# Kernel tuning notes

Hardware: AMD Instinct MI355X
Metric: run time of the kernel (lower is better)

The kernel has to match this reference:

```python
import jax, jax.numpy as jnp
import numpy as np

BS, RES = 2, 512
H_LVL = RES // 2 + 1   # floor(512/2)+1 = 257
W_LVL = RES            # 512
NQ = H_LVL * W_LVL     # 131584
D, HEADS, PTS = 128, 8, 4
DH = D // HEADS


def setup_inputs() -> dict:
    key = jax.random.key(0)
    ks = jax.random.split(key, 9)
    s = 0.02  # weight init scale
    return {
        "query":   jax.random.normal(ks[0], (BS, NQ, D), jnp.float32),
        "W_value": jax.random.normal(ks[1], (D, D), jnp.float32) * s,
        "b_value": jax.random.normal(ks[2], (D,), jnp.float32) * s,
        "W_off":   jax.random.normal(ks[3], (D, HEADS * PTS * 2), jnp.float32) * s,
        "b_off":   jax.random.normal(ks[4], (HEADS * PTS * 2,), jnp.float32) * s,
        "W_attn":  jax.random.normal(ks[5], (D, HEADS * PTS), jnp.float32) * s,
        "b_attn":  jax.random.normal(ks[6], (HEADS * PTS,), jnp.float32) * s,
        "W_out":   jax.random.normal(ks[7], (D, D), jnp.float32) * s,
        "b_out":   jax.random.normal(ks[8], (D,), jnp.float32) * s,
    }


def _bilinear_zeros(V, x, y, H, W):
    """grid_sample(mode=bilinear, padding=zeros, align_corners=False) equivalent.
    V: [G, H*W, DH]; x, y: [G, S] pixel coords. Returns [G, S, DH]."""
    x0 = jnp.floor(x); y0 = jnp.floor(y)
    x0i = x0.astype(jnp.int32); y0i = y0.astype(jnp.int32)
    x1i = x0i + 1; y1i = y0i + 1
    wx1 = x - x0; wx0 = 1.0 - wx1
    wy1 = y - y0; wy0 = 1.0 - wy1

    def corner(xi, yi, w):
        valid = (xi >= 0) & (xi < W) & (yi >= 0) & (yi < H)
        idx = jnp.clip(yi, 0, H - 1) * W + jnp.clip(xi, 0, W - 1)
        val = jnp.take_along_axis(V, idx[:, :, None], axis=1)  # [G,S,DH]
        return (w * valid.astype(w.dtype))[:, :, None] * val

    return (corner(x0i, y0i, wx0 * wy0) + corner(x1i, y0i, wx1 * wy0)
            + corner(x0i, y1i, wx0 * wy1) + corner(x1i, y1i, wx1 * wy1))


def reference(query, W_value, b_value, W_off, b_off, W_attn, b_attn, W_out, b_out):
    B, NQ_, D_ = query.shape
    H, W = H_LVL, W_LVL

    # projections (mmcv MSDeformAttn)
    value = (query @ W_value + b_value).reshape(B, NQ_, HEADS, DH)
    offsets = (query @ W_off + b_off).reshape(B, NQ_, HEADS, PTS, 2)  # num_levels=1
    attn = jax.nn.softmax((query @ W_attn + b_attn).reshape(B, NQ_, HEADS, PTS), axis=-1)

    # reference points: meshgrid of normalized (col=x, row=y), row-major flatten
    gy, gx = jnp.meshgrid(jnp.linspace(0.0, 1.0, H), jnp.linspace(0.0, 1.0, W), indexing="ij")
    ref = jnp.stack([gx, gy], axis=-1).reshape(NQ_, 2).astype(query.dtype)  # [NQ,2]

    # sampling locations in [0,1]; offset normalizer = (W, H)
    norm = jnp.array([W, H], dtype=query.dtype)
    loc = ref[None, :, None, None, :] + offsets / norm  # [B,NQ,HEADS,PTS,2]

    # grid_sample align_corners=False: pixel = loc*size - 0.5
    x = loc[..., 0] * W - 0.5
    y = loc[..., 1] * H - 0.5

    G = B * HEADS
    V = value.transpose(0, 2, 1, 3).reshape(G, H * W, DH)          # [G,HW,DH]
    xs = x.transpose(0, 2, 1, 3).reshape(G, NQ_ * PTS)
    ys = y.transpose(0, 2, 1, 3).reshape(G, NQ_ * PTS)

    samp = _bilinear_zeros(V, xs, ys, H, W).reshape(B, HEADS, NQ_, PTS, DH)
    aw = attn.transpose(0, 2, 1, 3)                                 # [B,HEADS,NQ,PTS]
    out = jnp.einsum("bhqp,bhqpd->bqhd", aw, samp).reshape(B, NQ_, D_)
    out = out @ W_out + b_out

    # mmcv adds identity inside the attention module; outer forward adds residual again
    return out + query + query
```

## Files before the change

### kernel.cpp

```cpp
#include <hip/hip_runtime.h>
#include <hip/hip_bf16.h>

#define BS     2
#define H_LVL  257
#define W_LVL  512
#define NQC    (H_LVL * W_LVL)
#define DD     128
#define HEADS  8
#define PTS    4
#define DH     16
#define MTOT   (BS * NQC)

typedef float v4f __attribute__((ext_vector_type(4)));
typedef short v8s __attribute__((ext_vector_type(8)));

static __device__ __forceinline__ unsigned short f2bb(float f) {
    union { float f; unsigned int u; } v; v.f = f;
    const unsigned int u = v.u;
    return (unsigned short)((u + 0x7fffu + ((u >> 16) & 1u)) >> 16);
}
static __device__ __forceinline__ float bb2f(unsigned short h) {
    union { unsigned int u; float f; } v; v.u = ((unsigned int)h) << 16;
    return v.f;
}
static __device__ __forceinline__ void fma4(float4& acc, float w, const unsigned short* p) {
    const ushort4 r = *(const ushort4*)p;
    acc.x = fmaf(w, bb2f(r.x), acc.x);
    acc.y = fmaf(w, bb2f(r.y), acc.y);
    acc.z = fmaf(w, bb2f(r.z), acc.z);
    acc.w = fmaf(w, bb2f(r.w), acc.w);
}

__global__ __launch_bounds__(256) void prep_kernel(
    const float* __restrict__ Wv, const float* __restrict__ Woff,
    const float* __restrict__ Wattn, const float* __restrict__ Wout,
    const float* __restrict__ boff, const float* __restrict__ battn,
    unsigned short* __restrict__ WtV, unsigned short* __restrict__ Wt96,
    unsigned short* __restrict__ WtO, float* __restrict__ bcat)
{
    const int id = blockIdx.x * 256 + threadIdx.x;
    {
        const int n = id >> 7, k = id & 127;
        WtV[id] = f2bb(Wv[k * DD + n]);
        WtO[id] = f2bb(Wout[k * DD + n]);
    }
    if (id < 96 * 128) {
        const int n = id >> 7, k = id & 127;
        Wt96[id] = f2bb(n < 64 ? Woff[k * 64 + n] : Wattn[k * 32 + (n - 64)]);
    }
    if (id < 96) bcat[id] = (id < 64) ? boff[id] : battn[id - 64];
}

template<int NT, int MODE>
__global__ __launch_bounds__(256) void gemm_kernel(
    const float* __restrict__ A,
    const unsigned short* __restrict__ Wt,
    const float* __restrict__ bias,
    unsigned short* __restrict__ dst_bf,
    float* __restrict__ dst_f,
    const float* __restrict__ query)
{
    constexpr int NC = NT * 16;
    __shared__ unsigned short As[64 * 136];
    __shared__ unsigned short Ws[NC * 136];
    const int t = threadIdx.x;
    const long long m0 = (long long)blockIdx.x * 64;

    {
        const float4* src = (const float4*)(A + m0 * DD);
        #pragma unroll
        for (int rep = 0; rep < 8; ++rep) {
            const int c = rep * 256 + t;
            const int m = c >> 5, f4 = c & 31;
            const float4 v = src[c];
            ushort4 hq;
            hq.x = f2bb(v.x); hq.y = f2bb(v.y); hq.z = f2bb(v.z); hq.w = f2bb(v.w);
            *(ushort4*)(&As[m * 136 + f4 * 4]) = hq;
        }
    }
    {
        const uint4* src = (const uint4*)Wt;
        for (int c = t; c < NC * 16; c += 256) {
            const int n = c >> 4, kc = c & 15;
            *(uint4*)(&Ws[n * 136 + kc * 8]) = src[c];
        }
    }
    __syncthreads();

    const int lane = t & 63, wave = t >> 6;
    const int l15 = lane & 15, quad = lane >> 4;

    v4f acc[NT];
    #pragma unroll
    for (int nt = 0; nt < NT; ++nt) { v4f z = {0.f, 0.f, 0.f, 0.f}; acc[nt] = z; }

    const int arow = wave * 16 + l15;
    #pragma unroll
    for (int kk = 0; kk < 4; ++kk) {
        const v8s a = *(const v8s*)(&As[arow * 136 + kk * 32 + quad * 8]);
        #pragma unroll
        for (int nt = 0; nt < NT; ++nt) {
            const v8s b = *(const v8s*)(&Ws[(nt * 16 + l15) * 136 + kk * 32 + quad * 8]);
            acc[nt] = __builtin_amdgcn_mfma_f32_16x16x32_bf16(a, b, acc[nt], 0, 0, 0);
        }
    }

    const long long mbase = m0 + wave * 16 + quad * 4;
    if (MODE == 0) {
        const int b = (int)(m0 / NQC);
        #pragma unroll
        for (int nt = 0; nt < NT; ++nt) {
            const float bi = bias[nt * 16 + l15];
            #pragma unroll
            for (int r = 0; r < 4; ++r) {
                const long long q = (mbase + r) - (long long)b * NQC;
                dst_bf[((long long)(b * HEADS + nt) * NQC + q) * DH + l15] =
                    f2bb(acc[nt][r] + bi);
            }
        }
    } else if (MODE == 1) {
        #pragma unroll
        for (int nt = 0; nt < NT; ++nt) {
            const float bi = bias[nt * 16 + l15];
            #pragma unroll
            for (int r = 0; r < 4; ++r)
                dst_bf[(mbase + r) * 96 + nt * 16 + l15] = f2bb(acc[nt][r] + bi);
        }
    } else {
        #pragma unroll
        for (int nt = 0; nt < NT; ++nt) {
            const float bi = bias[nt * 16 + l15];
            #pragma unroll
            for (int r = 0; r < 4; ++r) {
                const long long idx = (mbase + r) * DD + nt * 16 + l15;
                dst_f[idx] = acc[nt][r] + bi + 2.0f * query[idx];
            }
        }
    }
}

template<bool PRECOMP>
__global__ __launch_bounds__(256) void sample2_kernel(
    const unsigned short* __restrict__ proj,
    const float* __restrict__ query,
    const float* __restrict__ Woff, const float* __restrict__ boff,
    const float* __restrict__ Wattn, const float* __restrict__ battn,
    const unsigned short* __restrict__ value,
    float* __restrict__ attn_out)
{
    __shared__ float projF[8][96];
    const int t = threadIdx.x;
    const long long qbase = (long long)blockIdx.x * 8;

    if constexpr (PRECOMP) {
        if (t < 192) {
            const ushort4 r = *(const ushort4*)(proj + qbase * 96 + t * 4);
            const int qq = (t * 4) / 96, c = (t * 4) % 96;
            projF[qq][c]     = bb2f(r.x);
            projF[qq][c + 1] = bb2f(r.y);
            projF[qq][c + 2] = bb2f(r.z);
            projF[qq][c + 3] = bb2f(r.w);
        }
        __syncthreads();
    } else {
        __shared__ float qs[8][DD];
        {
            const int qi = t >> 5, k4 = (t & 31) * 4;
            const float4 v = *(const float4*)(query + (qbase + qi) * DD + k4);
            qs[qi][k4] = v.x; qs[qi][k4 + 1] = v.y; qs[qi][k4 + 2] = v.z; qs[qi][k4 + 3] = v.w;
        }
        __syncthreads();
        for (int task = t; task < 768; task += 256) {
            const int qi = task / 96, c = task % 96;
            float a; const float* wp; int stride;
            if (c < 64) { a = boff[c];       wp = Woff  + c;        stride = 64; }
            else        { a = battn[c - 64]; wp = Wattn + (c - 64); stride = 32; }
            for (int k = 0; k < DD; ++k) a += qs[qi][k] * wp[k * stride];
            projF[qi][c] = a;
        }
        __syncthreads();
    }

    const int q_loc = t >> 5, lq = t & 31;
    const int h = lq >> 2, p_own = lq & 3;
    const long long bq = qbase + q_loc;
    const int b = (int)(bq / NQC);
    const int qidx = (int)(bq - (long long)b * NQC);
    const int row = qidx >> 9, col = qidx & 511;

    const float offx = projF[q_loc][(h * PTS + p_own) * 2];
    const float offy = projF[q_loc][(h * PTS + p_own) * 2 + 1];
    const float al   = projF[q_loc][64 + h * PTS + p_own];
    float mx = fmaxf(al, __shfl_xor(al, 1));
    mx = fmaxf(mx, __shfl_xor(mx, 2));
    const float e = __expf(al - mx);
    float sm = e + __shfl_xor(e, 1);
    sm += __shfl_xor(sm, 2);
    const float aw = e / sm;

    const float x = (float)col * (1.0f / 511.0f) * (float)W_LVL + offx - 0.5f;
    const float y = (float)row * (1.0f / 256.0f) * (float)H_LVL + offy - 0.5f;
    const float x0f = floorf(x), y0f = floorf(y);
    const int x0 = (int)x0f, y0 = (int)y0f;
    const int x1 = x0 + 1, y1 = y0 + 1;
    const float wx1 = x - x0f, wx0 = 1.0f - wx1;
    const float wy1 = y - y0f, wy0 = 1.0f - wy1;
    const float vx0 = (x0 >= 0 && x0 < W_LVL) ? 1.f : 0.f;
    const float vx1 = (x1 >= 0 && x1 < W_LVL) ? 1.f : 0.f;
    const float vy0 = (y0 >= 0 && y0 < H_LVL) ? 1.f : 0.f;
    const float vy1 = (y1 >= 0 && y1 < H_LVL) ? 1.f : 0.f;
    float w00 = aw * wx0 * wy0 * vx0 * vy0;
    float w01 = aw * wx1 * wy0 * vx1 * vy0;
    float w10 = aw * wx0 * wy1 * vx0 * vy1;
    float w11 = aw * wx1 * wy1 * vx1 * vy1;
    const int xc0 = min(max(x0, 0), W_LVL - 1), xc1 = min(max(x1, 0), W_LVL - 1);
    const int yc0 = min(max(y0, 0), H_LVL - 1), yc1 = min(max(y1, 0), H_LVL - 1);
    int i00 = yc0 * W_LVL + xc0, i01 = yc0 * W_LVL + xc1;
    int i10 = yc1 * W_LVL + xc0, i11 = yc1 * W_LVL + xc1;

    const int dq4 = p_own;
    const unsigned short* V = value + (size_t)(b * HEADS + h) * NQC * DH + dq4 * 4;
    float4 acc = {0.f, 0.f, 0.f, 0.f};
    const int lbase = (t & 63) & ~3;
    #pragma unroll
    for (int p = 0; p < 4; ++p) {
        const int src = lbase + p;
        const float W00 = __shfl(w00, src, 64), W01 = __shfl(w01, src, 64);
        const float W10 = __shfl(w10, src, 64), W11 = __shfl(w11, src, 64);
        const int   I00 = __shfl(i00, src, 64), I01 = __shfl(i01, src, 64);
        const int   I10 = __shfl(i10, src, 64), I11 = __shfl(i11, src, 64);
        fma4(acc, W00, V + (size_t)I00 * DH);
        fma4(acc, W01, V + (size_t)I01 * DH);
        fma4(acc, W10, V + (size_t)I10 * DH);
        fma4(acc, W11, V + (size_t)I11 * DH);
    }
    *(float4*)(attn_out + bq * DD + h * DH + dq4 * 4) = acc;
}

extern "C" void kernel_launch(void* const* d_in, const int* in_sizes, int n_in,
                              void* d_out, int out_size, void* d_ws, size_t ws_size,
                              hipStream_t stream) {
    const float* query = (const float*)d_in[0];
    const float* Wv    = (const float*)d_in[1];
    const float* bv    = (const float*)d_in[2];
    const float* Woff  = (const float*)d_in[3];
    const float* boff  = (const float*)d_in[4];
    const float* Wattn = (const float*)d_in[5];
    const float* battn = (const float*)d_in[6];
    const float* Wout  = (const float*)d_in[7];
    const float* bout  = (const float*)d_in[8];
    float* out = (float*)d_out;

    char* ws = (char*)d_ws;
    size_t off = 0;
    unsigned short* WtV  = (unsigned short*)(ws + off); off += 16384 * 2;
    unsigned short* Wt96 = (unsigned short*)(ws + off); off += 12288 * 2;
    unsigned short* WtO  = (unsigned short*)(ws + off); off += 16384 * 2;
    float*          bcat = (float*)(ws + off);          off += 96 * 4;
    off = (off + 255) & ~(size_t)255;
    unsigned short* value = (unsigned short*)(ws + off);
    off += (size_t)BS * HEADS * NQC * DH * 2;
    off = (off + 255) & ~(size_t)255;
    unsigned short* proj = (unsigned short*)(ws + off);
    const size_t proj_need = (size_t)MTOT * 96 * 2;
    const bool precomp = (ws_size >= off + proj_need);

    prep_kernel<<<64, 256, 0, stream>>>(Wv, Woff, Wattn, Wout, boff, battn,
                                        WtV, Wt96, WtO, bcat);
    gemm_kernel<8, 0><<<MTOT / 64, 256, 0, stream>>>(query, WtV, bv, value, nullptr, nullptr);
    if (precomp) {
        gemm_kernel<6, 1><<<MTOT / 64, 256, 0, stream>>>(query, Wt96, bcat, proj, nullptr, nullptr);
        sample2_kernel<true><<<MTOT / 8, 256, 0, stream>>>(proj, nullptr, nullptr, nullptr,
                                                           nullptr, nullptr, value, out);
    } else {
        sample2_kernel<false><<<MTOT / 8, 256, 0, stream>>>(nullptr, query, Woff, boff,
                                                            Wattn, battn, value, out);
    }
    gemm_kernel<8, 2><<<MTOT / 64, 256, 0, stream>>>(out, WtO, bout, nullptr, out, query);
}
```

Baseline: 460.1 us.

## Fuse value and offset/attn projections into one GEMM; store sampled output as bf16

```diff
diff --git a/kernel.cpp b/kernel.cpp
--- a/kernel.cpp
+++ b/kernel.cpp
@@ -32,23 +32,104 @@
 }
 
 __global__ __launch_bounds__(256) void prep_kernel(
-    const float* __restrict__ Wv, const float* __restrict__ Woff,
-    const float* __restrict__ Wattn, const float* __restrict__ Wout,
-    const float* __restrict__ boff, const float* __restrict__ battn,
-    unsigned short* __restrict__ WtV, unsigned short* __restrict__ Wt96,
-    unsigned short* __restrict__ WtO, float* __restrict__ bcat)
+    const float* __restrict__ Wv, const float* __restrict__ bv,
+    const float* __restrict__ Woff, const float* __restrict__ boff,
+    const float* __restrict__ Wattn, const float* __restrict__ battn,
+    const float* __restrict__ Wout,
+    unsigned short* __restrict__ Wt224, unsigned short* __restrict__ WtO,
+    float* __restrict__ bcat224)
 {
     const int id = blockIdx.x * 256 + threadIdx.x;
     {
         const int n = id >> 7, k = id & 127;
-        WtV[id] = f2bb(Wv[k * DD + n]);
+        float v;
+        if (n < 128)      v = Wv[k * DD + n];
+        else if (n < 192) v = Woff[k * 64 + (n - 128)];
+        else              v = Wattn[k * 32 + (n - 192)];
+        Wt224[id] = f2bb(v);
+    }
+    if (id < 128 * 128) {
+        const int n = id >> 7, k = id & 127;
         WtO[id] = f2bb(Wout[k * DD + n]);
     }
-    if (id < 96 * 128) {
-        const int n = id >> 7, k = id & 127;
-        Wt96[id] = f2bb(n < 64 ? Woff[k * 64 + n] : Wattn[k * 32 + (n - 64)]);
-    }
-    if (id < 96) bcat[id] = (id < 64) ? boff[id] : battn[id - 64];
+    if (id < 224)
+        bcat224[id] = (id < 128) ? bv[id] : (id < 192 ? boff[id - 128] : battn[id - 192]);
+}
+
+__global__ __launch_bounds__(256) void gemm_fused_kernel(
+    const float* __restrict__ A,
+    const unsigned short* __restrict__ Wt,
+    const float* __restrict__ bias,
+    unsigned short* __restrict__ value,
+    unsigned short* __restrict__ proj)
+{
+    constexpr int NT = 14;
+    constexpr int NC = NT * 16;
+    __shared__ unsigned short As[64 * 136];
+    __shared__ unsigned short Ws[NC * 136];
+    const int t = threadIdx.x;
+    const long long m0 = (long long)blockIdx.x * 64;
+
+    {
+        const float4* src = (const float4*)(A + m0 * DD);
+        #pragma unroll
+        for (int rep = 0; rep < 8; ++rep) {
+            const int c = rep * 256 + t;
+            const int m = c >> 5, f4 = c & 31;
+            const float4 v = src[c];
+            ushort4 hq;
+            hq.x = f2bb(v.x); hq.y = f2bb(v.y); hq.z = f2bb(v.z); hq.w = f2bb(v.w);
+            *(ushort4*)(&As[m * 136 + f4 * 4]) = hq;
+        }
+    }
+    {
+        const uint4* src = (const uint4*)Wt;
+        #pragma unroll
+        for (int rep = 0; rep < 14; ++rep) {
+            const int c = rep * 256 + t;
+            const int n = c >> 4, kc = c & 15;
+            *(uint4*)(&Ws[n * 136 + kc * 8]) = src[c];
+        }
+    }
+    __syncthreads();
+
+    const int lane = t & 63, wave = t >> 6;
+    const int l15 = lane & 15, quad = lane >> 4;
+
+    v4f acc[NT];
+    #pragma unroll
+    for (int nt = 0; nt < NT; ++nt) { v4f z = {0.f, 0.f, 0.f, 0.f}; acc[nt] = z; }
+
+    const int arow = wave * 16 + l15;
+    #pragma unroll
+    for (int kk = 0; kk < 4; ++kk) {
+        const v8s a = *(const v8s*)(&As[arow * 136 + kk * 32 + quad * 8]);
+        #pragma unroll
+        for (int nt = 0; nt < NT; ++nt) {
+            const v8s b = *(const v8s*)(&Ws[(nt * 16 + l15) * 136 + kk * 32 + quad * 8]);
+            acc[nt] = __builtin_amdgcn_mfma_f32_16x16x32_bf16(a, b, acc[nt], 0, 0, 0);
+        }
+    }
+
+    const long long mbase = m0 + wave * 16 + quad * 4;
+    const int b = (int)(m0 / NQC);
+    #pragma unroll
+    for (int nt = 0; nt < 8; ++nt) {
+        const float bi = bias[nt * 16 + l15];
+        #pragma unroll
+        for (int r = 0; r < 4; ++r) {
+            const long long q = (mbase + r) - (long long)b * NQC;
+            value[((long long)(b * HEADS + nt) * NQC + q) * DH + l15] =
+                f2bb(acc[nt][r] + bi);
+        }
+    }
+    #pragma unroll
+    for (int nt = 8; nt < 14; ++nt) {
+        const float bi = bias[nt * 16 + l15];
+        #pragma unroll
+        for (int r = 0; r < 4; ++r)
+            proj[(mbase + r) * 96 + (nt - 8) * 16 + l15] = f2bb(acc[nt][r] + bi);
+    }
 }
 
 template<int NT, int MODE>
@@ -118,14 +199,6 @@
                     f2bb(acc[nt][r] + bi);
             }
         }
-    } else if (MODE == 1) {
-        #pragma unroll
-        for (int nt = 0; nt < NT; ++nt) {
-            const float bi = bias[nt * 16 + l15];
-            #pragma unroll
-            for (int r = 0; r < 4; ++r)
-                dst_bf[(mbase + r) * 96 + nt * 16 + l15] = f2bb(acc[nt][r] + bi);
-        }
     } else {
         #pragma unroll
         for (int nt = 0; nt < NT; ++nt) {
@@ -139,7 +212,70 @@
     }
 }
 
-template<bool PRECOMP>
+__global__ __launch_bounds__(256) void gemm_out_kernel(
+    const unsigned short* Abf,
+    const unsigned short* __restrict__ Wt,
+    const float* __restrict__ bias,
+    float* dst,
+    const float* __restrict__ query)
+{
+    constexpr int NT = 8;
+    __shared__ unsigned short As[64 * 136];
+    __shared__ unsigned short Ws[128 * 136];
+    const int t = threadIdx.x;
+    const long long m0 = (long long)blockIdx.x * 64;
+
+    {
+        const uint4* src = (const uint4*)((const char*)Abf + ((size_t)blockIdx.x << 15));
+        #pragma unroll
+        for (int rep = 0; rep < 4; ++rep) {
+            const int c = rep * 256 + t;
+            const int m = c >> 4, kc = c & 15;
+            *(uint4*)(&As[m * 136 + kc * 8]) = src[c];
+        }
+    }
+    {
+        const uint4* src = (const uint4*)Wt;
+        #pragma unroll
+        for (int rep = 0; rep < 8; ++rep) {
+            const int c = rep * 256 + t;
+            const int n = c >> 4, kc = c & 15;
+            *(uint4*)(&Ws[n * 136 + kc * 8]) = src[c];
+        }
+    }
+    __syncthreads();
+
+    const int lane = t & 63, wave = t >> 6;
+    const int l15 = lane & 15, quad = lane >> 4;
+
+    v4f acc[NT];
+    #pragma unroll
+    for (int nt = 0; nt < NT; ++nt) { v4f z = {0.f, 0.f, 0.f, 0.f}; acc[nt] = z; }
+
+    const int arow = wave * 16 + l15;
+    #pragma unroll
+    for (int kk = 0; kk < 4; ++kk) {
+        const v8s a = *(const v8s*)(&As[arow * 136 + kk * 32 + quad * 8]);
+        #pragma unroll
+        for (int nt = 0; nt < NT; ++nt) {
+            const v8s b = *(const v8s*)(&Ws[(nt * 16 + l15) * 136 + kk * 32 + quad * 8]);
+            acc[nt] = __builtin_amdgcn_mfma_f32_16x16x32_bf16(a, b, acc[nt], 0, 0, 0);
+        }
+    }
+
+    const long long mbase = m0 + wave * 16 + quad * 4;
+    #pragma unroll
+    for (int nt = 0; nt < NT; ++nt) {
+        const float bi = bias[nt * 16 + l15];
+        #pragma unroll
+        for (int r = 0; r < 4; ++r) {
+            const long long idx = (mbase + r) * DD + nt * 16 + l15;
+            dst[idx] = acc[nt][r] + bi + 2.0f * query[idx];
+        }
+    }
+}
+
+template<bool PRECOMP, bool BF16OUT>
 __global__ __launch_bounds__(256) void sample2_kernel(
     const unsigned short* __restrict__ proj,
     const float* __restrict__ query,
@@ -234,7 +370,15 @@
         fma4(acc, W10, V + (size_t)I10 * DH);
         fma4(acc, W11, V + (size_t)I11 * DH);
     }
-    *(float4*)(attn_out + bq * DD + h * DH + dq4 * 4) = acc;
+    if constexpr (BF16OUT) {
+        ushort4 h4;
+        h4.x = f2bb(acc.x); h4.y = f2bb(acc.y); h4.z = f2bb(acc.z); h4.w = f2bb(acc.w);
+        char* dstp = (char*)attn_out + (((size_t)(bq >> 6)) << 15)
+                   + (((size_t)(bq & 63)) << 8) + (size_t)(h * 32 + dq4 * 8);
+        *(ushort4*)dstp = h4;
+    } else {
+        *(float4*)(attn_out + bq * DD + h * DH + dq4 * 4) = acc;
+    }
 }
 
 extern "C" void kernel_launch(void* const* d_in, const int* in_sizes, int n_in,
@@ -253,10 +397,9 @@
 
     char* ws = (char*)d_ws;
     size_t off = 0;
-    unsigned short* WtV  = (unsigned short*)(ws + off); off += 16384 * 2;
-    unsigned short* Wt96 = (unsigned short*)(ws + off); off += 12288 * 2;
-    unsigned short* WtO  = (unsigned short*)(ws + off); off += 16384 * 2;
-    float*          bcat = (float*)(ws + off);          off += 96 * 4;
+    unsigned short* Wt224 = (unsigned short*)(ws + off); off += 224 * 128 * 2;
+    unsigned short* WtO   = (unsigned short*)(ws + off); off += 128 * 128 * 2;
+    float*          bcat  = (float*)(ws + off);          off += 224 * 4;
     off = (off + 255) & ~(size_t)255;
     unsigned short* value = (unsigned short*)(ws + off);
     off += (size_t)BS * HEADS * NQC * DH * 2;
@@ -265,16 +408,19 @@
     const size_t proj_need = (size_t)MTOT * 96 * 2;
     const bool precomp = (ws_size >= off + proj_need);
 
-    prep_kernel<<<64, 256, 0, stream>>>(Wv, Woff, Wattn, Wout, boff, battn,
-                                        WtV, Wt96, WtO, bcat);
-    gemm_kernel<8, 0><<<MTOT / 64, 256, 0, stream>>>(query, WtV, bv, value, nullptr, nullptr);
+    prep_kernel<<<112, 256, 0, stream>>>(Wv, bv, Woff, boff, Wattn, battn, Wout,
+                                         Wt224, WtO, bcat);
     if (precomp) {
-        gemm_kernel<6, 1><<<MTOT / 64, 256, 0, stream>>>(query, Wt96, bcat, proj, nullptr, nullptr);
-        sample2_kernel<true><<<MTOT / 8, 256, 0, stream>>>(proj, nullptr, nullptr, nullptr,
-                                                           nullptr, nullptr, value, out);
+        gemm_fused_kernel<<<MTOT / 64, 256, 0, stream>>>(query, Wt224, bcat, value, proj);
+        sample2_kernel<true, true><<<MTOT / 8, 256, 0, stream>>>(
+            proj, nullptr, nullptr, nullptr, nullptr, nullptr, value, out);
+        gemm_out_kernel<<<MTOT / 64, 256, 0, stream>>>(
+            (const unsigned short*)out, WtO, bout, out, query);
     } else {
-        sample2_kernel<false><<<MTOT / 8, 256, 0, stream>>>(nullptr, query, Woff, boff,
-                                                            Wattn, battn, value, out);
-    }
-    gemm_kernel<8, 2><<<MTOT / 64, 256, 0, stream>>>(out, WtO, bout, nullptr, out, query);
-}
+        gemm_kernel<8, 0><<<MTOT / 64, 256, 0, stream>>>(query, Wt224, bcat, value,
+                                                         nullptr, nullptr);
+        sample2_kernel<false, false><<<MTOT / 8, 256, 0, stream>>>(
+            nullptr, query, Woff, boff, Wattn, battn, value, out);
+        gemm_kernel<8, 2><<<MTOT / 64, 256, 0, stream>>>(out, WtO, bout, nullptr, out, query);
+    }
+}
```

Result: faster. 387.1 us (-15.9%).
